# Kernel optimization log

Hardware: AMD Instinct MI355X
Metric: run time of the kernel (lower is better)

## Reference

```python
import jax, jax.numpy as jnp
import numpy as np

B, S, D, H = 2, 2048, 1024, 16
HD = D // H  # head dim = 64


def setup_inputs() -> dict:
    key = jax.random.key(0)
    ks = jax.random.split(key, 9)
    sc = 1.0 / np.sqrt(D)
    x = jax.random.normal(ks[0], (B, S, D), dtype=jnp.float32)
    # weights stored as (in, out); y = x @ W + b (same math as torch Linear with W.T)
    Wq = jax.random.normal(ks[1], (D, D), dtype=jnp.float32) * sc
    Wk = jax.random.normal(ks[2], (D, D), dtype=jnp.float32) * sc
    Wv = jax.random.normal(ks[3], (D, D), dtype=jnp.float32) * sc
    Wo = jax.random.normal(ks[4], (D, D), dtype=jnp.float32) * sc
    bq = jax.random.normal(ks[5], (D,), dtype=jnp.float32) * 0.01
    bk = jax.random.normal(ks[6], (D,), dtype=jnp.float32) * 0.01
    bv = jax.random.normal(ks[7], (D,), dtype=jnp.float32) * 0.01
    bo = jax.random.normal(ks[8], (D,), dtype=jnp.float32) * 0.01
    return {"x": x, "Wq": Wq, "bq": bq, "Wk": Wk, "bk": bk,
            "Wv": Wv, "bv": bv, "Wo": Wo, "bo": bo}


def reference(x, Wq, bq, Wk, bk, Wv, bv, Wo, bo):
    b, s, d = x.shape
    q = (x @ Wq + bq).reshape(b, s, H, HD)
    k = (x @ Wk + bk).reshape(b, s, H, HD)
    v = (x @ Wv + bv).reshape(b, s, H, HD)
    # [b, h, s, s] scores, scaled by sqrt(head_dim)
    scores = jnp.einsum('bqhd,bkhd->bhqk', q, k) / np.sqrt(HD)
    causal = jnp.triu(jnp.ones((s, s), dtype=bool), k=1)  # True above diagonal
    scores = jnp.where(causal, -jnp.inf, scores)
    w = jax.nn.softmax(scores, axis=-1)  # dropout rate 0 -> identity
    ctx = jnp.einsum('bhqk,bkhd->bqhd', w, v).reshape(b, s, d)
    return ctx @ Wo + bo
```

## Files before the change

### kernel.cpp

```cpp
#include <hip/hip_runtime.h>
#include <math.h>

#define BB 2
#define SS 2048
#define DD 1024
#define HH 16
#define HDIM 64

typedef __bf16 bf16_t;
typedef __attribute__((ext_vector_type(8))) __bf16 bf16x8;
typedef __attribute__((ext_vector_type(4))) __bf16 bf16x4;
typedef __attribute__((ext_vector_type(4))) float f32x4;

__device__ inline bf16_t f2bf(float f) {
    unsigned int x; __builtin_memcpy(&x, &f, 4);
    unsigned int r = (x + 0x7FFFu + ((x >> 16) & 1u)) >> 16;
    unsigned short us = (unsigned short)r;
    bf16_t b; __builtin_memcpy(&b, &us, 2); return b;
}
__device__ inline unsigned int cvtpk(float a, float b) {
    unsigned int r;
    asm("v_cvt_pk_bf16_f32 %0, %1, %2" : "=v"(r) : "v"(a), "v"(b));
    return r;
}
__device__ inline void gload16(const void* g, void* lds_base) {
    __builtin_amdgcn_global_load_lds(
        (const __attribute__((address_space(1))) void*)g,
        (__attribute__((address_space(3))) void*)lds_base, 16, 0, 0);
}

#define SCL 0.18033688f
#define FM  12.0f

__global__ __launch_bounds__(256)
void prep_kernel(const float* __restrict__ x, bf16_t* __restrict__ xb,
                 const float* __restrict__ W0, const float* __restrict__ W1,
                 const float* __restrict__ W2, const float* __restrict__ W3,
                 bf16x8* __restrict__ P0, bf16x8* __restrict__ P1,
                 bf16x8* __restrict__ P2, bf16x8* __restrict__ P3) {
    const int bid = blockIdx.x, tid = threadIdx.x;
    if (bid < 2048) {
        const int i = bid * 512 + tid;
        #pragma unroll
        for (int u = 0; u < 2; ++u) {
            const int j = i + u * 256;
            const float4 v = reinterpret_cast<const float4*>(x)[j];
            bf16x4 o;
            o.x = f2bf(v.x); o.y = f2bf(v.y); o.z = f2bf(v.z); o.w = f2bf(v.w);
            reinterpret_cast<bf16x4*>(xb)[j] = o;
        }
    } else {
        const int t = (bid - 2048) * 256 + tid;
        const int g = t >> 10, n = t & 1023;
        const float* Ws[4] = {W0, W1, W2, W3};
        bf16x8* Pp[4] = {P0, P1, P2, P3};
        #pragma unroll
        for (int m = 0; m < 4; ++m) {
            bf16x8 v;
            #pragma unroll
            for (int j = 0; j < 8; ++j) v[j] = f2bf(Ws[m][(size_t)(g * 8 + j) * DD + n]);
            Pp[m][(size_t)g * DD + n] = v;
        }
    }
}

__global__ __launch_bounds__(256)
void gemm_qkv(const bf16_t* __restrict__ A,
              const bf16x8* __restrict__ Wp0, const bf16x8* __restrict__ Wp1,
              const bf16x8* __restrict__ Wp2,
              const float* __restrict__ b0, const float* __restrict__ b1,
              const float* __restrict__ b2,
              bf16_t* __restrict__ C0, bf16_t* __restrict__ C1,
              bf16_t* __restrict__ Vt) {
    __shared__ bf16x8 smem_v[3072];
    char* const smem = (char*)smem_v;

    const int f = blockIdx.x;
    const int xcd = f & 7, l = f >> 3;
    const int ytile = xcd * 4 + (l & 3);
    const int zx = l >> 2;
    const int z = zx >> 3;
    const int xtile = zx & 7;

    const bf16x8* Wp = (z == 0) ? Wp0 : (z == 1) ? Wp1 : Wp2;
    const float* bias = (z == 0) ? b0 : (z == 1) ? b1 : b2;

    const int tid = threadIdx.x;
    const int ln = tid & 63, wv = tid >> 6;
    const int quad = ln >> 4, l15 = ln & 15;
    const int wr = wv >> 1, wc = wv & 1;
    const int m0 = ytile * 128;
    const int n0 = xtile * 128;

    int arow[2], acl[2], bg[2], bn[2];
    #pragma unroll
    for (int u = 0; u < 2; ++u) {
        const int S = (wv * 2 + u) * 64 + ln;
        arow[u] = S >> 2; acl[u] = (S & 3) ^ ((arow[u] >> 1) & 3);
        bg[u] = S >> 7;   bn[u] = S & 127;
    }

    f32x4 acc[4][4];
    #pragma unroll
    for (int i = 0; i < 4; ++i)
        #pragma unroll
        for (int j = 0; j < 4; ++j) acc[i][j] = (f32x4){0.f, 0.f, 0.f, 0.f};

    auto stage = [&](int t, int buf) {
        char* const base = smem + buf * 16384;
        const int k0 = t * 32, kg0 = t * 4;
        #pragma unroll
        for (int u = 0; u < 2; ++u) {
            gload16(&A[(size_t)(m0 + arow[u]) * DD + k0 + acl[u] * 8],
                    base + (wv * 2 + u) * 1024);
            gload16(&Wp[(size_t)(kg0 + bg[u]) * DD + n0 + bn[u]],
                    base + 8192 + (wv * 2 + u) * 1024);
        }
    };

    stage(0, 0);
    stage(1, 1);
    asm volatile("s_waitcnt vmcnt(4)" ::: "memory");
    __builtin_amdgcn_s_barrier();

    #pragma unroll
    for (int t = 0; t < 32; ++t) {
        const int bsel = t % 3;
        const bf16x8 (*As)[4]   = reinterpret_cast<const bf16x8(*)[4]>(smem + bsel * 16384);
        const bf16x8 (*Bs)[128] = reinterpret_cast<const bf16x8(*)[128]>(smem + bsel * 16384 + 8192);
        bf16x8 fa[4], fb[4];
        #pragma unroll
        for (int mi = 0; mi < 4; ++mi) {
            const int row = wr * 64 + mi * 16 + l15;
            fa[mi] = As[row][quad ^ ((row >> 1) & 3)];
        }
        #pragma unroll
        for (int ni = 0; ni < 4; ++ni)
            fb[ni] = Bs[quad][wc * 64 + ni * 16 + l15];
        if (t + 2 < 32) stage(t + 2, (t + 2) % 3);
        #pragma unroll
        for (int mi = 0; mi < 4; ++mi)
            #pragma unroll
            for (int ni = 0; ni < 4; ++ni)
                acc[mi][ni] = __builtin_amdgcn_mfma_f32_16x16x32_bf16(
                    fa[mi], fb[ni], acc[mi][ni], 0, 0, 0);
        if (t < 30)       asm volatile("s_waitcnt vmcnt(4)" ::: "memory");
        else if (t == 30) asm volatile("s_waitcnt vmcnt(0)" ::: "memory");
        if (t < 31) __builtin_amdgcn_s_barrier();
    }

    if (z < 2) {
        bf16_t* C = (z == 0) ? C0 : C1;
        const float sc = (z == 0) ? SCL : 1.0f;
        #pragma unroll
        for (int ni = 0; ni < 4; ++ni) {
            const int col = n0 + wc * 64 + ni * 16 + l15;
            const float bv = bias[col];
            #pragma unroll
            for (int mi = 0; mi < 4; ++mi)
                #pragma unroll
                for (int r = 0; r < 4; ++r) {
                    const int row = m0 + wr * 64 + mi * 16 + quad * 4 + r;
                    C[(size_t)row * DD + col] = f2bf((acc[mi][ni][r] + bv) * sc);
                }
        }
    } else {
        unsigned short (*T)[136] = reinterpret_cast<unsigned short(*)[136]>(smem);
        __syncthreads();
        #pragma unroll
        for (int ni = 0; ni < 4; ++ni) {
            const int cl = wc * 64 + ni * 16 + l15;
            const float bv = bias[n0 + cl];
            #pragma unroll
            for (int mi = 0; mi < 4; ++mi) {
                const int rl = wr * 64 + mi * 16 + quad * 4;
                uint2 pk;
                pk.x = cvtpk(acc[mi][ni][0] + bv, acc[mi][ni][1] + bv);
                pk.y = cvtpk(acc[mi][ni][2] + bv, acc[mi][ni][3] + bv);
                *reinterpret_cast<uint2*>(&T[cl][rl]) = pk;
            }
        }
        __syncthreads();
        const int b = m0 >> 11, s0 = m0 & 2047, h0 = n0 >> 6;
        #pragma unroll
        for (int u = 0; u < 8; ++u) {
            const int c = u * 256 + tid;
            const int s8 = c & 15, nl = c >> 4;
            const bf16x8 v = *reinterpret_cast<const bf16x8*>(&T[nl][s8 * 8]);
            const int bh = b * 16 + h0 + (nl >> 6), d = nl & 63;
            *reinterpret_cast<bf16x8*>(
                &Vt[((size_t)bh * 64 + d) * SS + s0 + s8 * 8]) = v;
        }
    }
}

__global__ __launch_bounds__(256)
void gemm_out(const bf16_t* __restrict__ A, const bf16x8* __restrict__ Wp,
              const float* __restrict__ bias, float* __restrict__ C) {
    __shared__ bf16x8 smem_v[4608];
    char* const smem = (char*)smem_v;

    const int f = blockIdx.x;
    const int xcd = f & 7, l = f >> 3;
    const int ytile = xcd * 4 + (l & 3);
    const int xtile = l >> 2;

    const int tid = threadIdx.x;
    const int ln = tid & 63, wv = tid >> 6;
    const int quad = ln >> 4, l15 = ln & 15;
    const int wr = wv >> 1, wc = wv & 1;
    const int m0 = ytile * 128;
    const int n0 = xtile * 64;

    int arow[4], acl[4], bkg[2], bnn[2];
    #pragma unroll
    for (int u = 0; u < 4; ++u) {
        const int S = (wv * 4 + u) * 64 + ln;
        arow[u] = S >> 3; acl[u] = (S & 7) ^ (arow[u] & 7);
    }
    #pragma unroll
    for (int u = 0; u < 2; ++u) {
        const int S = (wv * 2 + u) * 64 + ln;
        bkg[u] = S >> 6; bnn[u] = S & 63;
    }

    f32x4 acc[4][2];
    #pragma unroll
    for (int i = 0; i < 4; ++i)
        #pragma unroll
        for (int j = 0; j < 2; ++j) acc[i][j] = (f32x4){0.f, 0.f, 0.f, 0.f};

    auto stage = [&](int t, int buf) {
        char* const base = smem + buf * 24576;
        const int k0 = t * 64, kg0 = t * 8;
        #pragma unroll
        for (int u = 0; u < 4; ++u)
            gload16(&A[(size_t)(m0 + arow[u]) * DD + k0 + acl[u] * 8],
                    base + (wv * 4 + u) * 1024);
        #pragma unroll
        for (int u = 0; u < 2; ++u)
            gload16(&Wp[(size_t)(kg0 + bkg[u]) * DD + n0 + bnn[u]],
                    base + 16384 + (wv * 2 + u) * 1024);
    };

    stage(0, 0);
    stage(1, 1);
    asm volatile("s_waitcnt vmcnt(6)" ::: "memory");
    __builtin_amdgcn_s_barrier();

    #pragma unroll
    for (int t = 0; t < 16; ++t) {
        const int bsel = t % 3;
        const bf16x8 (*As)[8] = reinterpret_cast<const bf16x8(*)[8]>(smem + bsel * 24576);
        const bf16x8 (*Bs)[64] = reinterpret_cast<const bf16x8(*)[64]>(smem + bsel * 24576 + 16384);
        bf16x8 fa[2][4], fb[2][2];
        #pragma unroll
        for (int kk = 0; kk < 2; ++kk) {
            #pragma unroll
            for (int mi = 0; mi < 4; ++mi) {
                const int row = wr * 64 + mi * 16 + l15;
                fa[kk][mi] = As[row][(kk * 4 + quad) ^ (row & 7)];
            }
            #pragma unroll
            for (int ni = 0; ni < 2; ++ni)
                fb[kk][ni] = Bs[kk * 4 + quad][wc * 32 + ni * 16 + l15];
        }
        if (t + 2 < 16) stage(t + 2, (t + 2) % 3);
        #pragma unroll
        for (int kk = 0; kk < 2; ++kk)
            #pragma unroll
            for (int mi = 0; mi < 4; ++mi)
                #pragma unroll
                for (int ni = 0; ni < 2; ++ni)
                    acc[mi][ni] = __builtin_amdgcn_mfma_f32_16x16x32_bf16(
                        fa[kk][mi], fb[kk][ni], acc[mi][ni], 0, 0, 0);
        if (t < 14)       asm volatile("s_waitcnt vmcnt(6)" ::: "memory");
        else if (t == 14) asm volatile("s_waitcnt vmcnt(0)" ::: "memory");
        if (t < 15) __builtin_amdgcn_s_barrier();
    }

    #pragma unroll
    for (int ni = 0; ni < 2; ++ni) {
        const int col = n0 + wc * 32 + ni * 16 + l15;
        const float bv = bias[col];
        #pragma unroll
        for (int mi = 0; mi < 4; ++mi)
            #pragma unroll
            for (int r = 0; r < 4; ++r) {
                const int row = m0 + wr * 64 + mi * 16 + quad * 4 + r;
                C[(size_t)row * DD + col] = acc[mi][ni][r] + bv;
            }
    }
}

__global__ __launch_bounds__(256)
void attn_mfma(const bf16_t* __restrict__ Q, const bf16_t* __restrict__ Kg,
               const bf16_t* __restrict__ Vt, bf16_t* __restrict__ Ctx) {
    __shared__ bf16x8 Ks[2][64][8];
    __shared__ bf16x8 Vs[2][64][8];
    __shared__ unsigned short Ps[4][16][64];

    const int tid = threadIdx.x;
    const int ln = tid & 63, w = tid >> 6;
    const int quad = ln >> 4, l15 = ln & 15;

    const int f = blockIdx.x;
    const int xcd = f & 7, l = f >> 3;
    const int bh = xcd * 4 + (l & 3);
    const int ytile = l >> 2;
    const int tswz = (bh + ytile) & 15;
    const int qt = (ytile < 16) ? tswz : 31 - tswz;

    const int b = bh >> 4, h = bh & 15;
    const size_t rowbase = (size_t)b * SS;
    const int col0 = h * 64;

    const int krow0 = w * 16 + (ln >> 3);
    const int krow1 = krow0 + 8;
    const int kc0 = (ln & 7) ^ (krow0 & 7);
    const int kc1 = (ln & 7) ^ (krow1 & 7);

    bf16x8 fq[2];
    const int qrow = qt * 64 + w * 16 + l15;
    #pragma unroll
    for (int kk = 0; kk < 2; ++kk)
        fq[kk] = *reinterpret_cast<const bf16x8*>(
            &Q[(rowbase + qrow) * DD + col0 + kk * 32 + quad * 8]);

    f32x4 acc_o[4];
    #pragma unroll
    for (int i = 0; i < 4; ++i) acc_o[i] = (f32x4){0.f, 0.f, 0.f, 0.f};
    float lsum = 0.f;

    const bf16_t* kp0 = &Kg[(rowbase + krow0) * DD + col0 + kc0 * 8];
    const bf16_t* kp1 = &Kg[(rowbase + krow1) * DD + col0 + kc1 * 8];
    const bf16_t* vp0 = &Vt[((size_t)bh * 64 + krow0) * SS + kc0 * 8];
    const bf16_t* vp1 = &Vt[((size_t)bh * 64 + krow1) * SS + kc1 * 8];

    auto stageadv = [&](int buf) {
        char* kb = (char*)Ks + buf * 8192 + w * 2048;
        char* vb = (char*)Vs + buf * 8192 + w * 2048;
        gload16(kp0, kb);
        gload16(kp1, kb + 1024);
        gload16(vp0, vb);
        gload16(vp1, vb + 1024);
        kp0 += 64 * DD; kp1 += 64 * DD;
        vp0 += 64;      vp1 += 64;
    };

    const int swz = l15 & 7;

    auto compute_tile = [&](int buf, int dq) {
        unsigned short* const psw = &Ps[w][l15][0];
        #pragma unroll
        for (int ni = 0; ni < 4; ++ni) {
            const int slot = ni * 4 + quad;
            unsigned short* pdst = psw + (((slot >> 1) ^ swz) * 8 + (slot & 1) * 4);
            const int g = ni * 16;
            if (g > dq) {
                *reinterpret_cast<uint2*>(pdst) = (uint2){0u, 0u};
                continue;
            }
            f32x4 st = (f32x4){-FM, -FM, -FM, -FM};
            const int krow = ni * 16 + l15;
            #pragma unroll
            for (int kk = 0; kk < 2; ++kk) {
                const bf16x8 fk = Ks[buf][krow][(kk * 4 + quad) ^ (krow & 7)];
                st = __builtin_amdgcn_mfma_f32_16x16x32_bf16(fk, fq[kk], st, 0, 0, 0);
            }
            float p[4];
            #pragma unroll
            for (int r = 0; r < 4; ++r) {
                p[r] = __builtin_amdgcn_exp2f(st[r]);
                if (g == dq && (quad * 4 + r) > l15) p[r] = 0.f;
            }
            lsum += (p[0] + p[1]) + (p[2] + p[3]);
            uint2 pk;
            pk.x = cvtpk(p[0], p[1]);
            pk.y = cvtpk(p[2], p[3]);
            *reinterpret_cast<uint2*>(pdst) = pk;
        }
        __builtin_amdgcn_s_setprio(1);
        #pragma unroll
        for (int kk = 0; kk < 2; ++kk) {
            const bf16x8 fp = *reinterpret_cast<const bf16x8*>(
                &Ps[w][l15][(((kk * 4 + quad) ^ swz) * 8)]);
            #pragma unroll
            for (int nd = 0; nd < 4; ++nd) {
                const int vrow = nd * 16 + l15;
                const bf16x8 fv = Vs[buf][vrow][(kk * 4 + quad) ^ (vrow & 7)];
                acc_o[nd] = __builtin_amdgcn_mfma_f32_16x16x32_bf16(fv, fp, acc_o[nd], 0, 0, 0);
            }
        }
        __builtin_amdgcn_s_setprio(0);
    };

    stageadv(0);
    __syncthreads();
    int t = 0;
    while (t + 2 <= qt) {
        stageadv(1);
        compute_tile(0, 112);
        __syncthreads();
        stageadv(0);
        compute_tile(1, 112);
        __syncthreads();
        t += 2;
    }
    if (t < qt) {
        stageadv(1);
        compute_tile(0, 112);
        __syncthreads();
        compute_tile(1, w * 16);
    } else {
        compute_tile(0, w * 16);
    }

    {
        float s = lsum;
        s += __shfl_xor(s, 16);
        s += __shfl_xor(s, 32);
        const float inv = 1.f / s;
        const size_t orow = (rowbase + qrow) * DD + col0;
        #pragma unroll
        for (int nd = 0; nd < 4; ++nd) {
            uint2 ov;
            ov.x = cvtpk(acc_o[nd][0] * inv, acc_o[nd][1] * inv);
            ov.y = cvtpk(acc_o[nd][2] * inv, acc_o[nd][3] * inv);
            *reinterpret_cast<uint2*>(&Ctx[orow + nd * 16 + quad * 4]) = ov;
        }
    }
}

extern "C" void kernel_launch(void* const* d_in, const int* in_sizes, int n_in,
                              void* d_out, int out_size, void* d_ws, size_t ws_size,
                              hipStream_t stream) {
    const float* x  = (const float*)d_in[0];
    const float* Wq = (const float*)d_in[1];
    const float* bq = (const float*)d_in[2];
    const float* Wk = (const float*)d_in[3];
    const float* bk = (const float*)d_in[4];
    const float* Wv = (const float*)d_in[5];
    const float* bv = (const float*)d_in[6];
    const float* Wo = (const float*)d_in[7];
    const float* bo = (const float*)d_in[8];
    float* out = (float*)d_out;

    const size_t M = (size_t)BB * SS;
    const size_t mat = M * DD;
    const size_t wsz = (size_t)DD * DD;

    bf16_t* ws = (bf16_t*)d_ws;
    bf16_t* xb   = ws;
    bf16_t* Wqp  = ws + mat;
    bf16_t* Wkp  = Wqp + wsz;
    bf16_t* Wvp  = Wkp + wsz;
    bf16_t* Wop  = Wvp + wsz;
    bf16_t* Qb   = Wop + wsz;
    bf16_t* Kb   = Qb + mat;
    bf16_t* Vtb  = Kb + mat;
    bf16_t* Ctxb = Vtb + mat;

    dim3 blk(256);
    hipLaunchKernelGGL(prep_kernel, dim3(2560), blk, 0, stream,
                       x, xb, Wq, Wk, Wv, Wo,
                       (bf16x8*)Wqp, (bf16x8*)Wkp, (bf16x8*)Wvp, (bf16x8*)Wop);

    hipLaunchKernelGGL(gemm_qkv, dim3(768), blk, 0, stream,
                       xb, (const bf16x8*)Wqp, (const bf16x8*)Wkp, (const bf16x8*)Wvp,
                       bq, bk, bv, Qb, Kb, Vtb);

    hipLaunchKernelGGL(attn_mfma, dim3(1024), blk, 0, stream,
                       Qb, Kb, Vtb, Ctxb);

    hipLaunchKernelGGL(gemm_out, dim3(512), blk, 0, stream,
                       Ctxb, (const bf16x8*)Wop, bo, out);
}
```

Measured before the change: 168.5 us.

## Use two-wave 128-thread blocks with 64x128 warp tiles in QKV GEMM

Result: slower. 172.5 us (+2.4%).

```diff
diff --git a/kernel.cpp b/kernel.cpp
--- a/kernel.cpp
+++ b/kernel.cpp
@@ -64,7 +64,7 @@
     }
 }
 
-__global__ __launch_bounds__(256)
+__global__ __launch_bounds__(128, 2)
 void gemm_qkv(const bf16_t* __restrict__ A,
               const bf16x8* __restrict__ Wp0, const bf16x8* __restrict__ Wp1,
               const bf16x8* __restrict__ Wp2,
@@ -88,39 +88,38 @@
     const int tid = threadIdx.x;
     const int ln = tid & 63, wv = tid >> 6;
     const int quad = ln >> 4, l15 = ln & 15;
-    const int wr = wv >> 1, wc = wv & 1;
     const int m0 = ytile * 128;
     const int n0 = xtile * 128;
 
-    int arow[2], acl[2], bg[2], bn[2];
-    #pragma unroll
-    for (int u = 0; u < 2; ++u) {
-        const int S = (wv * 2 + u) * 64 + ln;
+    int arow[4], acl[4], bg[4], bn[4];
+    #pragma unroll
+    for (int u = 0; u < 4; ++u) {
+        const int S = u * 128 + tid;
         arow[u] = S >> 2; acl[u] = (S & 3) ^ ((arow[u] >> 1) & 3);
         bg[u] = S >> 7;   bn[u] = S & 127;
     }
 
-    f32x4 acc[4][4];
+    f32x4 acc[4][8];
     #pragma unroll
     for (int i = 0; i < 4; ++i)
         #pragma unroll
-        for (int j = 0; j < 4; ++j) acc[i][j] = (f32x4){0.f, 0.f, 0.f, 0.f};
+        for (int j = 0; j < 8; ++j) acc[i][j] = (f32x4){0.f, 0.f, 0.f, 0.f};
 
     auto stage = [&](int t, int buf) {
         char* const base = smem + buf * 16384;
         const int k0 = t * 32, kg0 = t * 4;
         #pragma unroll
-        for (int u = 0; u < 2; ++u) {
+        for (int u = 0; u < 4; ++u) {
             gload16(&A[(size_t)(m0 + arow[u]) * DD + k0 + acl[u] * 8],
-                    base + (wv * 2 + u) * 1024);
+                    base + u * 2048 + wv * 1024);
             gload16(&Wp[(size_t)(kg0 + bg[u]) * DD + n0 + bn[u]],
-                    base + 8192 + (wv * 2 + u) * 1024);
+                    base + 8192 + u * 2048 + wv * 1024);
         }
     };
 
     stage(0, 0);
     stage(1, 1);
-    asm volatile("s_waitcnt vmcnt(4)" ::: "memory");
+    asm volatile("s_waitcnt vmcnt(8)" ::: "memory");
     __builtin_amdgcn_s_barrier();
 
     #pragma unroll
@@ -128,23 +127,23 @@
         const int bsel = t % 3;
         const bf16x8 (*As)[4]   = reinterpret_cast<const bf16x8(*)[4]>(smem + bsel * 16384);
         const bf16x8 (*Bs)[128] = reinterpret_cast<const bf16x8(*)[128]>(smem + bsel * 16384 + 8192);
-        bf16x8 fa[4], fb[4];
+        bf16x8 fa[4], fb[8];
         #pragma unroll
         for (int mi = 0; mi < 4; ++mi) {
-            const int row = wr * 64 + mi * 16 + l15;
+            const int row = wv * 64 + mi * 16 + l15;
             fa[mi] = As[row][quad ^ ((row >> 1) & 3)];
         }
         #pragma unroll
-        for (int ni = 0; ni < 4; ++ni)
-            fb[ni] = Bs[quad][wc * 64 + ni * 16 + l15];
+        for (int ni = 0; ni < 8; ++ni)
+            fb[ni] = Bs[quad][ni * 16 + l15];
         if (t + 2 < 32) stage(t + 2, (t + 2) % 3);
         #pragma unroll
         for (int mi = 0; mi < 4; ++mi)
             #pragma unroll
-            for (int ni = 0; ni < 4; ++ni)
+            for (int ni = 0; ni < 8; ++ni)
                 acc[mi][ni] = __builtin_amdgcn_mfma_f32_16x16x32_bf16(
                     fa[mi], fb[ni], acc[mi][ni], 0, 0, 0);
-        if (t < 30)       asm volatile("s_waitcnt vmcnt(4)" ::: "memory");
+        if (t < 30)       asm volatile("s_waitcnt vmcnt(8)" ::: "memory");
         else if (t == 30) asm volatile("s_waitcnt vmcnt(0)" ::: "memory");
         if (t < 31) __builtin_amdgcn_s_barrier();
     }
@@ -153,14 +152,14 @@
         bf16_t* C = (z == 0) ? C0 : C1;
         const float sc = (z == 0) ? SCL : 1.0f;
         #pragma unroll
-        for (int ni = 0; ni < 4; ++ni) {
-            const int col = n0 + wc * 64 + ni * 16 + l15;
+        for (int ni = 0; ni < 8; ++ni) {
+            const int col = n0 + ni * 16 + l15;
             const float bv = bias[col];
             #pragma unroll
             for (int mi = 0; mi < 4; ++mi)
                 #pragma unroll
                 for (int r = 0; r < 4; ++r) {
-                    const int row = m0 + wr * 64 + mi * 16 + quad * 4 + r;
+                    const int row = m0 + wv * 64 + mi * 16 + quad * 4 + r;
                     C[(size_t)row * DD + col] = f2bf((acc[mi][ni][r] + bv) * sc);
                 }
         }
@@ -168,12 +167,12 @@
         unsigned short (*T)[136] = reinterpret_cast<unsigned short(*)[136]>(smem);
         __syncthreads();
         #pragma unroll
-        for (int ni = 0; ni < 4; ++ni) {
-            const int cl = wc * 64 + ni * 16 + l15;
+        for (int ni = 0; ni < 8; ++ni) {
+            const int cl = ni * 16 + l15;
             const float bv = bias[n0 + cl];
             #pragma unroll
             for (int mi = 0; mi < 4; ++mi) {
-                const int rl = wr * 64 + mi * 16 + quad * 4;
+                const int rl = wv * 64 + mi * 16 + quad * 4;
                 uint2 pk;
                 pk.x = cvtpk(acc[mi][ni][0] + bv, acc[mi][ni][1] + bv);
                 pk.y = cvtpk(acc[mi][ni][2] + bv, acc[mi][ni][3] + bv);
@@ -183,8 +182,8 @@
         __syncthreads();
         const int b = m0 >> 11, s0 = m0 & 2047, h0 = n0 >> 6;
         #pragma unroll
-        for (int u = 0; u < 8; ++u) {
-            const int c = u * 256 + tid;
+        for (int u = 0; u < 16; ++u) {
+            const int c = u * 128 + tid;
             const int s8 = c & 15, nl = c >> 4;
             const bf16x8 v = *reinterpret_cast<const bf16x8*>(&T[nl][s8 * 8]);
             const int bh = b * 16 + h0 + (nl >> 6), d = nl & 63;
@@ -461,18 +460,17 @@
     bf16_t* Vtb  = Kb + mat;
     bf16_t* Ctxb = Vtb + mat;
 
-    dim3 blk(256);
-    hipLaunchKernelGGL(prep_kernel, dim3(2560), blk, 0, stream,
+    hipLaunchKernelGGL(prep_kernel, dim3(2560), dim3(256), 0, stream,
                        x, xb, Wq, Wk, Wv, Wo,
                        (bf16x8*)Wqp, (bf16x8*)Wkp, (bf16x8*)Wvp, (bf16x8*)Wop);
 
-    hipLaunchKernelGGL(gemm_qkv, dim3(768), blk, 0, stream,
+    hipLaunchKernelGGL(gemm_qkv, dim3(768), dim3(128), 0, stream,
                        xb, (const bf16x8*)Wqp, (const bf16x8*)Wkp, (const bf16x8*)Wvp,
                        bq, bk, bv, Qb, Kb, Vtb);
 
-    hipLaunchKernelGGL(attn_mfma, dim3(1024), blk, 0, stream,
+    hipLaunchKernelGGL(attn_mfma, dim3(1024), dim3(256), 0, stream,
                        Qb, Kb, Vtb, Ctxb);
 
-    hipLaunchKernelGGL(gemm_out, dim3(512), blk, 0, stream,
+    hipLaunchKernelGGL(gemm_out, dim3(512), dim3(256), 0, stream,
                        Ctxb, (const bf16x8*)Wop, bo, out);
 }
```
